# Performance work log

Hardware: AMD Instinct MI355X
Metric: run time of the kernel (lower is better)

## Reference

```python
import jax, jax.numpy as jnp
import numpy as np

B, S, H2 = 32, 4096, 512  # H2 = 2*hidden_size


def setup_inputs() -> dict:
    key = jax.random.key(0)
    ks = jax.random.split(key, 10)
    s = 1.0 / np.sqrt(H2)
    return {
        "decoder_state": jax.random.normal(ks[0], (B, 1, H2), jnp.float32),
        "encoder_outputs": jax.random.normal(ks[1], (B, S, H2), jnp.float32),
        "coverage_vector": jax.random.uniform(ks[2], (B, S, H2), jnp.float32),
        "W_h": jax.random.uniform(ks[3], (H2, H2), jnp.float32, -s, s),
        "b_h": jax.random.uniform(ks[4], (H2,), jnp.float32, -s, s),
        "W_s": jax.random.uniform(ks[5], (H2, H2), jnp.float32, -s, s),
        "b_s": jax.random.uniform(ks[6], (H2,), jnp.float32, -s, s),
        "W_c": jax.random.uniform(ks[7], (H2, H2), jnp.float32, -s, s),
        "b_c": jax.random.uniform(ks[8], (H2,), jnp.float32, -s, s),
        "v": jax.random.uniform(ks[9], (H2, 1), jnp.float32, -s, s),
    }


def reference(decoder_state, encoder_outputs, coverage_vector,
              W_h, b_h, W_s, b_s, W_c, b_c, v):
    # additive attention features: [B, S, 2H]
    e = jnp.tanh(encoder_outputs @ W_h + b_h
                 + decoder_state @ W_s + b_s      # broadcasts over S
                 + coverage_vector @ W_c + b_c)
    scores = e @ v                                # [B, S, 1]
    attn_dist = jax.nn.softmax(scores, axis=1)    # softmax over source positions
    # weighted sum of encoder outputs: [B, 1, 2H]
    h_star_t = jnp.einsum('bsi,bsd->bid', attn_dist, encoder_outputs)
    coverage_new = coverage_vector + attn_dist    # broadcast over feature dim
    return h_star_t, attn_dist, coverage_new
```

## Files before the change

### kernel.cpp

```cpp
#include <hip/hip_runtime.h>
#include <hip/hip_bf16.h>
#include <stdint.h>

#define H2    512
#define BATCH 32
#define SEQ   4096
#define BM    64
#define BKS   32
#define NKT3  32

typedef __attribute__((ext_vector_type(4))) float f32x4;
typedef __attribute__((ext_vector_type(8))) short bf16x8;

typedef __attribute__((address_space(3))) unsigned int       as3_uint;
typedef const __attribute__((address_space(1))) unsigned int as1_uint;

__device__ __forceinline__ unsigned short f2bf(float f) {
    union { float f; unsigned u; } v; v.f = f;
    unsigned r = v.u + 0x7FFF + ((v.u >> 16) & 1);
    return (unsigned short)(r >> 16);
}

__device__ __forceinline__ float fast_tanh(float x) {
    float e = __builtin_amdgcn_exp2f(x * 2.88539008177793f);
    return 1.0f - 2.0f * __builtin_amdgcn_rcpf(e + 1.0f);
}

__global__ void kprep_w(const float* __restrict__ Wh, const float* __restrict__ Wc,
                        unsigned short* __restrict__ wt) {
    int c    = blockIdx.x * blockDim.x + threadIdx.x;
    int lane = c & 63;
    int cb   = (c >> 6) & 31;
    int kt   = c >> 11;
    int col  = cb * 16 + (lane & 15);
    int k0   = kt * 32 + (lane >> 4) * 8;
    unsigned short tmp[8];
#pragma unroll
    for (int j = 0; j < 8; ++j) {
        int kg = k0 + j;
        float w = (kg < 512) ? Wh[kg * 512 + col] : Wc[(kg - 512) * 512 + col];
        tmp[j] = f2bf(w);
    }
    *reinterpret_cast<uint4*>(wt + (size_t)c * 8) = *reinterpret_cast<const uint4*>(tmp);
}

__global__ void kprep_q(const float* __restrict__ dec, const float* __restrict__ Ws,
                        const float* __restrict__ bh, const float* __restrict__ bs,
                        const float* __restrict__ bc, float* __restrict__ q) {
    __shared__ float dsh[512];
    int b = blockIdx.x, t = threadIdx.x;
    dsh[t]       = dec[b * 512 + t];
    dsh[t + 256] = dec[b * 512 + 256 + t];
    __syncthreads();
    float a0 = 0.f, a1 = 0.f;
#pragma unroll 4
    for (int k = 0; k < 512; ++k) {
        float d = dsh[k];
        a0 = fmaf(d, Ws[k * 512 + t], a0);
        a1 = fmaf(d, Ws[k * 512 + 256 + t], a1);
    }
    q[b * 512 + t]       = a0 + bh[t] + bs[t] + bc[t];
    q[b * 512 + 256 + t] = a1 + bh[256 + t] + bs[256 + t] + bc[256 + t];
}

__launch_bounds__(512, 4)
__global__ void kgemm(const float* __restrict__ enc, const float* __restrict__ cov,
                      const unsigned short* __restrict__ wt,
                      const float* __restrict__ q, const float* __restrict__ vvec,
                      float* __restrict__ scores) {
    extern __shared__ char lds[];
    unsigned short* Bsm = (unsigned short*)lds;
    unsigned short* Asm = (unsigned short*)(lds + 65536);

    int tid  = threadIdx.x;
    int lane = tid & 63, wn = tid >> 6;

    int cpx  = gridDim.x >> 3;
    int swz  = (blockIdx.x & 7) * cpx + (blockIdx.x >> 3);
    int row0 = swz * BM;

    int r = tid >> 2, k8 = tid & 3;
    const float* aeb = enc + (size_t)(row0 + r) * H2 + k8 * 8;
    const float* acb = cov + (size_t)(row0 + r) * H2 + k8 * 8;
    unsigned awb = (unsigned)((r >> 4) * 1024 + k8 * 256 +
                              (((r & 15) * 16) ^ (k8 << 4)));
    unsigned arb = (unsigned)((lane >> 4) * 256 +
                              (((lane & 15) * 16) ^ ((lane >> 4) << 4)));
    unsigned brb = (unsigned)(wn * 4096 + lane * 16);
    const unsigned short* gsrc = wt + ((size_t)wn * 4 * 64 + lane) * 8;

    f32x4 acc[4][4] = {};
    f32x4 pA0, pA1;

    if (tid < 256) {
        pA0 = *reinterpret_cast<const f32x4*>(aeb);
        pA1 = *reinterpret_cast<const f32x4*>(aeb + 4);
    }
#pragma unroll
    for (int i = 0; i < 4; ++i)
        __builtin_amdgcn_global_load_lds(
            (as1_uint*)(gsrc + (size_t)i * 512),
            (as3_uint*)((char*)Bsm + wn * 4096 + i * 1024), 16, 0, 0);
    if (tid < 256) {
        union { unsigned short h[8]; uint4 u; } u;
#pragma unroll
        for (int j = 0; j < 4; ++j) { u.h[j] = f2bf(pA0[j]); u.h[4 + j] = f2bf(pA1[j]); }
        *reinterpret_cast<uint4*>((char*)Asm + awb) = u.u;
    }
    asm volatile("s_waitcnt lgkmcnt(0)" ::: "memory");
    __builtin_amdgcn_sched_barrier(0);
    __builtin_amdgcn_s_barrier();
    __builtin_amdgcn_sched_barrier(0);

#pragma unroll 2
    for (int t = 0; t < NKT3; ++t) {
        const int cur = t & 1, nxt = cur ^ 1;
        asm volatile("s_waitcnt vmcnt(0)" ::: "memory");
        __builtin_amdgcn_sched_barrier(0);
        if (t + 1 < NKT3 && tid < 256) {
            const float* src = (t + 1 < 16) ? (aeb + (t + 1) * 32)
                                            : (acb + (t - 15) * 32);
            pA0 = *reinterpret_cast<const f32x4*>(src);
            pA1 = *reinterpret_cast<const f32x4*>(src + 4);
        }
        bf16x8 af[4], bf[4];
#pragma unroll
        for (int mi = 0; mi < 4; ++mi)
            af[mi] = *reinterpret_cast<const bf16x8*>(
                (char*)Asm + cur * 4096 + mi * 1024 + arb);
#pragma unroll
        for (int ni = 0; ni < 4; ++ni)
            bf[ni] = *reinterpret_cast<const bf16x8*>(
                (char*)Bsm + cur * 32768 + ni * 1024 + brb);
        if (t + 1 < NKT3) {
            const unsigned short* gs = gsrc + (size_t)(t + 1) * 32 * 64 * 8;
#pragma unroll
            for (int i = 0; i < 4; ++i)
                __builtin_amdgcn_global_load_lds(
                    (as1_uint*)(gs + (size_t)i * 512),
                    (as3_uint*)((char*)Bsm + nxt * 32768 + wn * 4096 + i * 1024),
                    16, 0, 0);
        }
        __builtin_amdgcn_sched_barrier(0);
        __builtin_amdgcn_s_setprio(1);
#pragma unroll
        for (int mi = 0; mi < 4; ++mi)
#pragma unroll
            for (int ni = 0; ni < 4; ++ni)
                acc[mi][ni] = __builtin_amdgcn_mfma_f32_16x16x32_bf16(
                    af[mi], bf[ni], acc[mi][ni], 0, 0, 0);
        __builtin_amdgcn_s_setprio(0);
        if (t + 1 < NKT3 && tid < 256) {
            union { unsigned short h[8]; uint4 u; } u;
#pragma unroll
            for (int j = 0; j < 4; ++j) { u.h[j] = f2bf(pA0[j]); u.h[4 + j] = f2bf(pA1[j]); }
            *reinterpret_cast<uint4*>((char*)Asm + nxt * 4096 + awb) = u.u;
        }
        asm volatile("s_waitcnt lgkmcnt(0)" ::: "memory");
        __builtin_amdgcn_sched_barrier(0);
        __builtin_amdgcn_s_barrier();
        __builtin_amdgcn_sched_barrier(0);
    }

    float* qv   = (float*)lds;
    float* vv   = qv + 512;
    float* sred = vv + 512;
    qv[tid] = q[(row0 >> 12) * H2 + tid];
    vv[tid] = vvec[tid];
    __syncthreads();

    float ps[4][4] = {};
#pragma unroll
    for (int mi = 0; mi < 4; ++mi)
#pragma unroll
        for (int ni = 0; ni < 4; ++ni) {
            int colg = wn * 64 + ni * 16 + (lane & 15);
            float qq = qv[colg], vl = vv[colg];
#pragma unroll
            for (int j = 0; j < 4; ++j) {
                float e = fast_tanh(acc[mi][ni][j] + qq);
                ps[mi][j] = fmaf(e, vl, ps[mi][j]);
            }
        }
#pragma unroll
    for (int mi = 0; mi < 4; ++mi)
#pragma unroll
        for (int j = 0; j < 4; ++j) {
            float s = ps[mi][j];
            s += __shfl_xor(s, 1);
            s += __shfl_xor(s, 2);
            s += __shfl_xor(s, 4);
            s += __shfl_xor(s, 8);
            if ((lane & 15) == 0)
                sred[(mi * 16 + (lane >> 4) * 4 + j) * 8 + wn] = s;
        }
    __syncthreads();
    if (tid < BM) {
        float s = 0.f;
#pragma unroll
        for (int w = 0; w < 8; ++w) s += sred[tid * 8 + w];
        scores[row0 + tid] = s;
    }
}

__global__ void ksoftmax(const float* __restrict__ scores, float* __restrict__ out) {
    __shared__ float redm[16];
    __shared__ float reds[16];
    int b = blockIdx.x, t = threadIdx.x, lane = t & 63, w = t >> 6;
    if (t < 512) out[b * 512 + t] = 0.0f;
    f32x4 sv = *reinterpret_cast<const f32x4*>(scores + b * 4096 + t * 4);
    float m = fmaxf(fmaxf(sv[0], sv[1]), fmaxf(sv[2], sv[3]));
#pragma unroll
    for (int o = 1; o < 64; o <<= 1) m = fmaxf(m, __shfl_xor(m, o));
    if (lane == 0) redm[w] = m;
    __syncthreads();
    float mm = redm[0];
#pragma unroll
    for (int i = 1; i < 16; ++i) mm = fmaxf(mm, redm[i]);

    f32x4 p;
#pragma unroll
    for (int j = 0; j < 4; ++j)
        p[j] = __builtin_amdgcn_exp2f((sv[j] - mm) * 1.4426950408889634f);
    float s = p[0] + p[1] + p[2] + p[3];
#pragma unroll
    for (int o = 1; o < 64; o <<= 1) s += __shfl_xor(s, o);
    if (lane == 0) reds[w] = s;
    __syncthreads();
    float tot = 0.f;
#pragma unroll
    for (int i = 0; i < 16; ++i) tot += reds[i];
    float rinv = __builtin_amdgcn_rcpf(tot);
    p *= rinv;
    *reinterpret_cast<f32x4*>(out + 16384 + b * 4096 + t * 4) = p;
}

__global__ void kcov(const float* __restrict__ enc, const float* __restrict__ cov,
                     float* __restrict__ out) {
    const float* attn = out + 16384;
    float* covn  = out + 16384 + 131072;
    float* hstar = out;
    int blk = blockIdx.x;
    int b = blk >> 6, ck = blk & 63;
    int s0 = ck * 64;
    int t  = threadIdx.x;
    int f4 = (t & 127) * 4;
    int rp = t >> 7;
    size_t base = (size_t)b * SEQ * H2;
    f32x4 h = {0.f, 0.f, 0.f, 0.f};
#pragma unroll 2
    for (int i = 0; i < 32; ++i) {
        int s = s0 + i * 2 + rp;
        float a = attn[b * 4096 + s];
        size_t idx = base + (size_t)s * H2 + f4;
        f32x4 e4 = *reinterpret_cast<const f32x4*>(enc + idx);
        f32x4 c4 = *reinterpret_cast<const f32x4*>(cov + idx);
        c4 += a;
        __builtin_nontemporal_store(c4, reinterpret_cast<f32x4*>(covn + idx));
        h += a * e4;
    }
    int off = b * 512 + f4;
    atomicAdd(&hstar[off + 0], h[0]);
    atomicAdd(&hstar[off + 1], h[1]);
    atomicAdd(&hstar[off + 2], h[2]);
    atomicAdd(&hstar[off + 3], h[3]);
}

extern "C" void kernel_launch(void* const* d_in, const int* in_sizes, int n_in,
                              void* d_out, int out_size, void* d_ws, size_t ws_size,
                              hipStream_t stream) {
    const float* dec = (const float*)d_in[0];
    const float* enc = (const float*)d_in[1];
    const float* cov = (const float*)d_in[2];
    const float* Wh  = (const float*)d_in[3];
    const float* bh  = (const float*)d_in[4];
    const float* Ws  = (const float*)d_in[5];
    const float* bs  = (const float*)d_in[6];
    const float* Wc  = (const float*)d_in[7];
    const float* bc  = (const float*)d_in[8];
    const float* v   = (const float*)d_in[9];
    float* out = (float*)d_out;

    char* ws = (char*)d_ws;
    unsigned short* wt = (unsigned short*)ws;
    float* q      = (float*)(ws + (1 << 20));
    float* scores = (float*)(ws + (1 << 20) + 65536);

    static bool attr_done = false;
    if (!attr_done) {
        hipFuncSetAttribute((const void*)kgemm,
                            hipFuncAttributeMaxDynamicSharedMemorySize, 73728);
        attr_done = true;
    }

    kprep_w <<<dim3(256),  dim3(256),  0,     stream>>>(Wh, Wc, wt);
    kprep_q <<<dim3(32),   dim3(256),  0,     stream>>>(dec, Ws, bh, bs, bc, q);
    kgemm   <<<dim3(2048), dim3(512),  73728, stream>>>(enc, cov, wt, q, v, scores);
    ksoftmax<<<dim3(32),   dim3(1024), 0,     stream>>>(scores, out);
    kcov    <<<dim3(2048), dim3(256),  0,     stream>>>(enc, cov, out);
}
```

Measured before the change: 414.8 us.

## Prefetch A two tiles ahead, spread A loads across all threads, use packed bf16 convert

Restructures the GEMM main loop so all 512 threads load 4 floats of the A tile (instead of 256 threads loading 8), and the A global loads are issued two k-tiles ahead in a register double buffer, waited with vmcnt(1) instead of vmcnt(0). The B global-to-LDS loads are issued at the top of each iteration, and the last two iterations are peeled. The scalar float-to-bf16 rounding is replaced with the hardware v_cvt_pk_bf16_f32 instruction. The aim is to hide global latency behind the MFMAs and cut conversion ALU work, at the cost of more registers and more complex wait-count reasoning.

```diff
diff --git a/kernel.cpp b/kernel.cpp
--- a/kernel.cpp
+++ b/kernel.cpp
@@ -6,7 +6,6 @@
 #define BATCH 32
 #define SEQ   4096
 #define BM    64
-#define BKS   32
 #define NKT3  32
 
 typedef __attribute__((ext_vector_type(4))) float f32x4;
@@ -19,6 +18,13 @@
     union { float f; unsigned u; } v; v.f = f;
     unsigned r = v.u + 0x7FFF + ((v.u >> 16) & 1);
     return (unsigned short)(r >> 16);
+}
+
+__device__ __forceinline__ uint2 cvt4_bf16(f32x4 a) {
+    uint2 r;
+    asm("v_cvt_pk_bf16_f32 %0, %1, %2" : "=v"(r.x) : "v"(a[0]), "v"(a[1]));
+    asm("v_cvt_pk_bf16_f32 %0, %1, %2" : "=v"(r.y) : "v"(a[2]), "v"(a[3]));
+    return r;
 }
 
 __device__ __forceinline__ float fast_tanh(float x) {
@@ -79,92 +85,109 @@
     int swz  = (blockIdx.x & 7) * cpx + (blockIdx.x >> 3);
     int row0 = swz * BM;
 
-    int r = tid >> 2, k8 = tid & 3;
-    const float* aeb = enc + (size_t)(row0 + r) * H2 + k8 * 8;
-    const float* acb = cov + (size_t)(row0 + r) * H2 + k8 * 8;
-    unsigned awb = (unsigned)((r >> 4) * 1024 + k8 * 256 +
-                              (((r & 15) * 16) ^ (k8 << 4)));
+    int r = tid >> 3, k4 = tid & 7;
+    const float* aeb = enc + (size_t)(row0 + r) * H2 + k4 * 4;
+    const float* acb = cov + (size_t)(row0 + r) * H2 + k4 * 4;
+    unsigned awb = (unsigned)((r >> 4) * 1024 + (k4 >> 1) * 256 +
+                              (((r & 15) * 16) ^ ((k4 >> 1) << 4)) + (k4 & 1) * 8);
     unsigned arb = (unsigned)((lane >> 4) * 256 +
                               (((lane & 15) * 16) ^ ((lane >> 4) << 4)));
     unsigned brb = (unsigned)(wn * 4096 + lane * 16);
     const unsigned short* gsrc = wt + ((size_t)wn * 4 * 64 + lane) * 8;
 
     f32x4 acc[4][4] = {};
-    f32x4 pA0, pA1;
-
-    if (tid < 256) {
-        pA0 = *reinterpret_cast<const f32x4*>(aeb);
-        pA1 = *reinterpret_cast<const f32x4*>(aeb + 4);
-    }
-#pragma unroll
-    for (int i = 0; i < 4; ++i)
-        __builtin_amdgcn_global_load_lds(
-            (as1_uint*)(gsrc + (size_t)i * 512),
-            (as3_uint*)((char*)Bsm + wn * 4096 + i * 1024), 16, 0, 0);
-    if (tid < 256) {
-        union { unsigned short h[8]; uint4 u; } u;
-#pragma unroll
-        for (int j = 0; j < 4; ++j) { u.h[j] = f2bf(pA0[j]); u.h[4 + j] = f2bf(pA1[j]); }
-        *reinterpret_cast<uint4*>((char*)Asm + awb) = u.u;
-    }
-    asm volatile("s_waitcnt lgkmcnt(0)" ::: "memory");
+    f32x4 pA[2];
+
+#define ISSUE_B(T, BUF)                                                         \
+    {                                                                           \
+        const unsigned short* gs = gsrc + (size_t)(T) * 16384;                  \
+        _Pragma("unroll")                                                       \
+        for (int i = 0; i < 4; ++i)                                             \
+            __builtin_amdgcn_global_load_lds(                                   \
+                (as1_uint*)(gs + (size_t)i * 512),                              \
+                (as3_uint*)((char*)Bsm + (BUF) * 32768 + wn * 4096 + i * 1024), \
+                16, 0, 0);                                                      \
+    }
+#define A_SRC(T) (((T) < 16) ? (aeb + (T) * 32) : (acb + ((T) - 16) * 32))
+#define DS_READS(BUF, AF, BF)                                                   \
+    _Pragma("unroll")                                                           \
+    for (int mi = 0; mi < 4; ++mi)                                              \
+        AF[mi] = *reinterpret_cast<const bf16x8*>(                              \
+            (char*)Asm + (BUF) * 4096 + mi * 1024 + arb);                       \
+    _Pragma("unroll")                                                           \
+    for (int ni = 0; ni < 4; ++ni)                                              \
+        BF[ni] = *reinterpret_cast<const bf16x8*>(                              \
+            (char*)Bsm + (BUF) * 32768 + ni * 1024 + brb);
+#define MFMAS(AF, BF)                                                           \
+    __builtin_amdgcn_s_setprio(1);                                              \
+    _Pragma("unroll")                                                           \
+    for (int mi = 0; mi < 4; ++mi)                                              \
+        _Pragma("unroll")                                                       \
+        for (int ni = 0; ni < 4; ++ni)                                          \
+            acc[mi][ni] = __builtin_amdgcn_mfma_f32_16x16x32_bf16(              \
+                AF[mi], BF[ni], acc[mi][ni], 0, 0, 0);                          \
+    __builtin_amdgcn_s_setprio(0);
+#define STAGE_A(PAR, BUF)                                                       \
+    {                                                                           \
+        uint2 u = cvt4_bf16(pA[PAR]);                                           \
+        *reinterpret_cast<uint2*>((char*)Asm + (BUF) * 4096 + awb) = u;         \
+    }
+#define FENCE_BAR                                                               \
+    asm volatile("s_waitcnt lgkmcnt(0)" ::: "memory");                          \
+    __builtin_amdgcn_sched_barrier(0);                                          \
+    __builtin_amdgcn_s_barrier();                                               \
     __builtin_amdgcn_sched_barrier(0);
-    __builtin_amdgcn_s_barrier();
+
+    ISSUE_B(0, 0)
     __builtin_amdgcn_sched_barrier(0);
+    f32x4 a0 = *reinterpret_cast<const f32x4*>(A_SRC(0));
+    pA[1]    = *reinterpret_cast<const f32x4*>(A_SRC(1));
+    __builtin_amdgcn_sched_barrier(0);
+    {
+        uint2 u = cvt4_bf16(a0);
+        *reinterpret_cast<uint2*>((char*)Asm + awb) = u;
+    }
+    FENCE_BAR
 
 #pragma unroll 2
-    for (int t = 0; t < NKT3; ++t) {
+    for (int t = 0; t < NKT3 - 2; ++t) {
         const int cur = t & 1, nxt = cur ^ 1;
+        asm volatile("s_waitcnt vmcnt(1)" ::: "memory");
+        __builtin_amdgcn_sched_barrier(0);
+        ISSUE_B(t + 1, nxt)
+        __builtin_amdgcn_sched_barrier(0);
+        pA[cur] = *reinterpret_cast<const f32x4*>(A_SRC(t + 2));
+        __builtin_amdgcn_sched_barrier(0);
+        bf16x8 af[4], bf[4];
+        DS_READS(cur, af, bf)
+        MFMAS(af, bf)
+        STAGE_A(nxt, nxt)
+        FENCE_BAR
+    }
+
+    {
+        asm volatile("s_waitcnt vmcnt(1)" ::: "memory");
+        __builtin_amdgcn_sched_barrier(0);
+        ISSUE_B(31, 1)
+        __builtin_amdgcn_sched_barrier(0);
+        bf16x8 af[4], bf[4];
+        DS_READS(0, af, bf)
+        MFMAS(af, bf)
+        STAGE_A(1, 1)
+        FENCE_BAR
+    }
+    {
         asm volatile("s_waitcnt vmcnt(0)" ::: "memory");
         __builtin_amdgcn_sched_barrier(0);
-        if (t + 1 < NKT3 && tid < 256) {
-            const float* src = (t + 1 < 16) ? (aeb + (t + 1) * 32)
-                                            : (acb + (t - 15) * 32);
-            pA0 = *reinterpret_cast<const f32x4*>(src);
-            pA1 = *reinterpret_cast<const f32x4*>(src + 4);
-        }
         bf16x8 af[4], bf[4];
-#pragma unroll
-        for (int mi = 0; mi < 4; ++mi)
-            af[mi] = *reinterpret_cast<const bf16x8*>(
-                (char*)Asm + cur * 4096 + mi * 1024 + arb);
-#pragma unroll
-        for (int ni = 0; ni < 4; ++ni)
-            bf[ni] = *reinterpret_cast<const bf16x8*>(
-                (char*)Bsm + cur * 32768 + ni * 1024 + brb);
-        if (t + 1 < NKT3) {
-            const unsigned short* gs = gsrc + (size_t)(t + 1) * 32 * 64 * 8;
-#pragma unroll
-            for (int i = 0; i < 4; ++i)
-                __builtin_amdgcn_global_load_lds(
-                    (as1_uint*)(gs + (size_t)i * 512),
-                    (as3_uint*)((char*)Bsm + nxt * 32768 + wn * 4096 + i * 1024),
-                    16, 0, 0);
-        }
-        __builtin_amdgcn_sched_barrier(0);
-        __builtin_amdgcn_s_setprio(1);
-#pragma unroll
-        for (int mi = 0; mi < 4; ++mi)
-#pragma unroll
-            for (int ni = 0; ni < 4; ++ni)
-                acc[mi][ni] = __builtin_amdgcn_mfma_f32_16x16x32_bf16(
-                    af[mi], bf[ni], acc[mi][ni], 0, 0, 0);
-        __builtin_amdgcn_s_setprio(0);
-        if (t + 1 < NKT3 && tid < 256) {
-            union { unsigned short h[8]; uint4 u; } u;
-#pragma unroll
-            for (int j = 0; j < 4; ++j) { u.h[j] = f2bf(pA0[j]); u.h[4 + j] = f2bf(pA1[j]); }
-            *reinterpret_cast<uint4*>((char*)Asm + nxt * 4096 + awb) = u.u;
-        }
-        asm volatile("s_waitcnt lgkmcnt(0)" ::: "memory");
-        __builtin_amdgcn_sched_barrier(0);
-        __builtin_amdgcn_s_barrier();
-        __builtin_amdgcn_sched_barrier(0);
+        DS_READS(1, af, bf)
+        MFMAS(af, bf)
     }
 
     float* qv   = (float*)lds;
     float* vv   = qv + 512;
     float* sred = vv + 512;
+    __builtin_amdgcn_s_barrier();
     qv[tid] = q[(row0 >> 12) * H2 + tid];
     vv[tid] = vvec[tid];
     __syncthreads();
@@ -201,6 +224,12 @@
         for (int w = 0; w < 8; ++w) s += sred[tid * 8 + w];
         scores[row0 + tid] = s;
     }
+#undef ISSUE_B
+#undef A_SRC
+#undef DS_READS
+#undef MFMAS
+#undef STAGE_A
+#undef FENCE_BAR
 }
 
 __global__ void ksoftmax(const float* __restrict__ scores, float* __restrict__ out) {
```

Measured after the change: 403.9 us. 2.6% less time.
